# Performance work log

Measured on AMD Instinct MI355X. Metric: run time of the kernel, lower is better.

The kernel has to match this reference:

```python
import jax, jax.numpy as jnp
import numpy as np

B, S = 4, 2000            # meshes, nodes per mesh
N = B * S                  # total nodes
E = 32000                  # directed edges (before self loops)
H_TR, D_TR, FF, TOUT = 4, 64, 2048, 16
HID, HEADS, HC = 512, 6, 512
DEFORM_IN, NUM_LOOP = 7, 3


def setup_inputs():
    key = jax.random.key(0)
    ks = iter(jax.random.split(key, 64))
    def W(shape):
        return jax.random.normal(next(ks), shape, jnp.float32) / np.sqrt(shape[-1])
    inp = {}
    inp['conv_feat'] = jax.random.normal(next(ks), (B, 1), jnp.float32)
    inp['mesh_feat'] = jax.random.normal(next(ks), (N, 4), jnp.float32)
    inp['x'] = jax.random.normal(next(ks), (N, DEFORM_IN), jnp.float32)
    inp['edge_index'] = jax.random.randint(next(ks), (2, E), 0, N, jnp.int32)
    inp['embed_w'] = W((D_TR, 4)); inp['embed_b'] = jnp.zeros((D_TR,), jnp.float32)
    inp['in_proj_w'] = W((3 * D_TR, D_TR)); inp['in_proj_b'] = jnp.zeros((3 * D_TR,), jnp.float32)
    inp['out_proj_w'] = W((D_TR, D_TR)); inp['out_proj_b'] = jnp.zeros((D_TR,), jnp.float32)
    inp['ln1_g'] = jnp.ones((D_TR,), jnp.float32); inp['ln1_b'] = jnp.zeros((D_TR,), jnp.float32)
    inp['ln2_g'] = jnp.ones((D_TR,), jnp.float32); inp['ln2_b'] = jnp.zeros((D_TR,), jnp.float32)
    inp['ff1_w'] = W((FF, D_TR)); inp['ff1_b'] = jnp.zeros((FF,), jnp.float32)
    inp['ff2_w'] = W((D_TR, FF)); inp['ff2_b'] = jnp.zeros((D_TR,), jnp.float32)
    inp['tout_w'] = W((TOUT, D_TR)); inp['tout_b'] = jnp.zeros((TOUT,), jnp.float32)
    all_feat = DEFORM_IN - 2 + TOUT  # 21
    inp['lin_w'] = W((HID, all_feat)); inp['lin_b'] = jnp.zeros((HID,), jnp.float32)
    gin = 2 + HID  # 514
    inp['gat_wl'] = W((HEADS * HC, gin)); inp['gat_bl'] = jnp.zeros((HEADS * HC,), jnp.float32)
    inp['gat_wr'] = W((HEADS * HC, gin)); inp['gat_br'] = jnp.zeros((HEADS * HC,), jnp.float32)
    inp['gat_att'] = jax.random.normal(next(ks), (HEADS, HC), jnp.float32) / np.sqrt(HC)
    inp['gat_bias'] = jnp.zeros((HC,), jnp.float32)
    inp['coord1_w'] = W((HID // 2, HID)); inp['coord1_b'] = jnp.zeros((HID // 2,), jnp.float32)
    inp['coord2_w'] = W((2, HID // 2)); inp['coord2_b'] = jnp.zeros((2,), jnp.float32)
    return inp


def _ln(h, g, b):
    m = jnp.mean(h, -1, keepdims=True)
    v = jnp.var(h, -1, keepdims=True)
    return (h - m) / jnp.sqrt(v + 1e-5) * g + b


def _mrt_forward(conv_feat, mesh_feat, x, edge_index, embed_w, embed_b, in_proj_w, in_proj_b,
                 out_proj_w, out_proj_b, ln1_g, ln1_b, ln2_g, ln2_b, ff1_w, ff1_b, ff2_w, ff2_b,
                 tout_w, tout_b, lin_w, lin_b, gat_wl, gat_bl, gat_wr, gat_br, gat_att, gat_bias,
                 coord1_w, coord1_b, coord2_w, coord2_b):
    bsz = conv_feat.shape[0]
    feat_dim = mesh_feat.shape[-1]
    # ---- transformer encoder (1 post-norm layer, eval mode => no dropout) ----
    h = mesh_feat.reshape(bsz, -1, feat_dim) @ embed_w.T + embed_b  # [B,S,D]
    qkv = h @ in_proj_w.T + in_proj_b
    q, k, v = jnp.split(qkv, 3, axis=-1)
    dh = D_TR // H_TR
    hd = lambda t: t.reshape(bsz, -1, H_TR, dh)
    attn = jax.nn.softmax(jnp.einsum('bqhd,bkhd->bhqk', hd(q), hd(k)) / np.sqrt(dh), axis=-1)
    o = jnp.einsum('bhqk,bkhd->bqhd', attn, hd(v)).reshape(bsz, -1, D_TR)
    h = _ln(h + (o @ out_proj_w.T + out_proj_b), ln1_g, ln1_b)
    ff = jax.nn.relu(h @ ff1_w.T + ff1_b) @ ff2_w.T + ff2_b
    h = _ln(h + ff, ln2_g, ln2_b)
    feats = (h @ tout_w.T + tout_b).reshape(-1, TOUT)               # [N,16]
    feats = jnp.concatenate([x[:, 2:], feats], axis=1)             # [N,21]
    hidden = jax.nn.selu(feats @ lin_w.T + lin_b)                  # [N,512]
    # ---- recurrent GATv2 deformer loop ----
    coord = x[:, :2]
    n = x.shape[0]
    loops = jnp.arange(n, dtype=edge_index.dtype)                  # self loops (GATv2Conv default)
    src = jnp.concatenate([edge_index[0], loops])
    dst = jnp.concatenate([edge_index[1], loops])
    for _ in range(NUM_LOOP):
        inp = jnp.concatenate([coord, hidden], axis=1)             # [N,514]
        xl = (inp @ gat_wl.T + gat_bl).reshape(n, HEADS, HC)
        xr = (inp @ gat_wr.T + gat_br).reshape(n, HEADS, HC)
        e = jax.nn.leaky_relu(xl[src] + xr[dst], 0.2)              # [Etot,H,C]
        logits = jnp.einsum('ehc,hc->eh', e, gat_att)              # [Etot,H]
        mx = jax.ops.segment_max(logits, dst, num_segments=n)
        a = jnp.exp(logits - mx[dst])
        a = a / jax.ops.segment_sum(a, dst, num_segments=n)[dst]   # softmax per dst node
        agg = jax.ops.segment_sum(xl[src] * a[:, :, None], dst, num_segments=n)  # [N,H,C]
        hidden = jax.nn.selu(jnp.mean(agg, axis=1) + gat_bias)     # concat=False => head mean
        coord = jax.nn.selu(hidden @ coord1_w.T + coord1_b) @ coord2_w.T + coord2_b
    return coord


def reference(conv_feat, mesh_feat, x, edge_index, embed_w, embed_b, in_proj_w, in_proj_b,
              out_proj_w, out_proj_b, ln1_g, ln1_b, ln2_g, ln2_b, ff1_w, ff1_b, ff2_w, ff2_b,
              tout_w, tout_b, lin_w, lin_b, gat_wl, gat_bl, gat_wr, gat_br, gat_att, gat_bias,
              coord1_w, coord1_b, coord2_w, coord2_b):
    return _mrt_forward(conv_feat, mesh_feat, x, edge_index, embed_w, embed_b, in_proj_w, in_proj_b,
                        out_proj_w, out_proj_b, ln1_g, ln1_b, ln2_g, ln2_b, ff1_w, ff1_b, ff2_w, ff2_b,
                        tout_w, tout_b, lin_w, lin_b, gat_wl, gat_bl, gat_wr, gat_br, gat_att, gat_bias,
                        coord1_w, coord1_b, coord2_w, coord2_b)
```

## Files before the change

### kernel.cpp

```cpp
#include <hip/hip_runtime.h>
#include <hip/hip_bf16.h>
#include <math.h>

#define NN     8000
#define MPAD   8064
#define BATCH  4
#define SEQ    2000
#define DTR    64
#define NHTR   4
#define DHD    16
#define FFD    2048
#define TOUTD  16
#define HIDD   512
#define NHEADS 6
#define HCD    512
#define GIND   514
#define GOUT   3072
#define GOUT2  6144
#define NEDGE  32000
#define ELOOP  40000

#define K1     576
#define K2     1152

#define KSPLIT 20
#define KCH    100

#define CDIV(a,b) (((a)+(b)-1)/(b))

using bf16x8 = __attribute__((__ext_vector_type__(8))) __bf16;
using f32x4  = __attribute__((__ext_vector_type__(4))) float;

__device__ __forceinline__ float selu_f(float x){
  const float a = 1.6732632423543772848f;
  const float s = 1.0507009873554805f;
  return x > 0.f ? s * x : s * a * (__expf(x) - 1.f);
}

__device__ __forceinline__ unsigned short f2bf_rn(float x){
  unsigned u = __float_as_uint(x);
  unsigned r = (u + 0x7fffu + ((u >> 16) & 1u)) >> 16;
  return (unsigned short)r;
}
__device__ __forceinline__ float bf2f(unsigned short h){
  return __uint_as_float((unsigned)h << 16);
}

template<int ACT>
__global__ __launch_bounds__(256) void k_gemm(const float* __restrict__ A,
    const float* __restrict__ W, const float* __restrict__ bias,
    float* __restrict__ C, int M, int N, int K)
{
  __shared__ float As[16][68];
  __shared__ float Ws[16][68];
  const int tid = threadIdx.x;
  const int bm = blockIdx.y * 64, bn = blockIdx.x * 64;
  const int tx = tid & 15, ty = tid >> 4;
  float acc[4][4] = {};
  for (int k0 = 0; k0 < K; k0 += 16){
    #pragma unroll
    for (int i = 0; i < 4; ++i){
      int el = tid + (i << 8);
      int kk = el & 15, r = el >> 4;
      int gk = k0 + kk;
      int gm = bm + r;
      As[kk][r] = (gm < M && gk < K) ? A[(size_t)gm * K + gk] : 0.f;
      int gn = bn + r;
      Ws[kk][r] = (gn < N && gk < K) ? W[(size_t)gn * K + gk] : 0.f;
    }
    __syncthreads();
    #pragma unroll
    for (int kk = 0; kk < 16; ++kk){
      float av[4], wv[4];
      #pragma unroll
      for (int i = 0; i < 4; ++i) av[i] = As[kk][ty*4+i];
      #pragma unroll
      for (int j = 0; j < 4; ++j) wv[j] = Ws[kk][tx*4+j];
      #pragma unroll
      for (int i = 0; i < 4; ++i)
        #pragma unroll
        for (int j = 0; j < 4; ++j) acc[i][j] = fmaf(av[i], wv[j], acc[i][j]);
    }
    __syncthreads();
  }
  #pragma unroll
  for (int i = 0; i < 4; ++i){
    int gm = bm + ty*4 + i;
    if (gm >= M) continue;
    #pragma unroll
    for (int j = 0; j < 4; ++j){
      int gn = bn + tx*4 + j;
      if (gn >= N) continue;
      float v = acc[i][j] + bias[gn];
      if (ACT == 1) v = fmaxf(v, 0.f);
      if (ACT == 2) v = selu_f(v);
      C[(size_t)gm * N + gn] = v;
    }
  }
}

__global__ __launch_bounds__(256) void k_gemm_sk(const float* __restrict__ A,
    const float* __restrict__ W, float* __restrict__ part,
    int M, int N, int K, int kchunk)
{
  __shared__ float As[16][68];
  __shared__ float Ws[16][68];
  const int tid = threadIdx.x;
  const int bm = blockIdx.y * 64, bn = blockIdx.x * 64;
  const int kbeg = blockIdx.z * kchunk;
  const int tx = tid & 15, ty = tid >> 4;
  float acc[4][4] = {};
  for (int k0 = kbeg; k0 < kbeg + kchunk; k0 += 16){
    #pragma unroll
    for (int i = 0; i < 4; ++i){
      int el = tid + (i << 8);
      int kk = el & 15, r = el >> 4;
      int gk = k0 + kk;
      int gm = bm + r;
      As[kk][r] = (gm < M && gk < K) ? A[(size_t)gm * K + gk] : 0.f;
      int gn = bn + r;
      Ws[kk][r] = (gn < N && gk < K) ? W[(size_t)gn * K + gk] : 0.f;
    }
    __syncthreads();
    #pragma unroll
    for (int kk = 0; kk < 16; ++kk){
      float av[4], wv[4];
      #pragma unroll
      for (int i = 0; i < 4; ++i) av[i] = As[kk][ty*4+i];
      #pragma unroll
      for (int j = 0; j < 4; ++j) wv[j] = Ws[kk][tx*4+j];
      #pragma unroll
      for (int i = 0; i < 4; ++i)
        #pragma unroll
        for (int j = 0; j < 4; ++j) acc[i][j] = fmaf(av[i], wv[j], acc[i][j]);
    }
    __syncthreads();
  }
  float* pz = part + (size_t)blockIdx.z * M * N;
  #pragma unroll
  for (int i = 0; i < 4; ++i){
    int gm = bm + ty*4 + i;
    if (gm >= M) continue;
    #pragma unroll
    for (int j = 0; j < 4; ++j){
      int gn = bn + tx*4 + j;
      if (gn >= N) continue;
      pz[(size_t)gm * N + gn] = acc[i][j];
    }
  }
}

__global__ __launch_bounds__(256) void k_addln8(const float* __restrict__ x,
    const float* __restrict__ part, const float* __restrict__ bias,
    const float* __restrict__ g, const float* __restrict__ b,
    float* __restrict__ out)
{
  int row = blockIdx.x * 4 + (threadIdx.x >> 6);
  int lane = threadIdx.x & 63;
  if (row >= NN) return;
  float y = bias[lane];
  #pragma unroll
  for (int z = 0; z < 8; ++z) y += part[(size_t)z*NN*DTR + (size_t)row*64 + lane];
  float v = x[(size_t)row*64 + lane] + y;
  float s1 = v, s2 = v * v;
  #pragma unroll
  for (int o = 32; o; o >>= 1){ s1 += __shfl_xor(s1, o); s2 += __shfl_xor(s2, o); }
  float mean = s1 * (1.f/64.f);
  float var  = s2 * (1.f/64.f) - mean * mean;
  float r = rsqrtf(var + 1e-5f);
  out[(size_t)row*64 + lane] = (v - mean) * r * g[lane] + b[lane];
}

__global__ __launch_bounds__(256) void k_coord2(const float* __restrict__ c1,
    const float* __restrict__ w2, const float* __restrict__ b2,
    float* __restrict__ out, short* __restrict__ abf)
{
  int n = blockIdx.x, t = threadIdx.x;
  float v = c1[(size_t)n*256 + t];
  float d0 = v * w2[t], d1 = v * w2[256 + t];
  #pragma unroll
  for (int o = 32; o; o >>= 1){ d0 += __shfl_xor(d0, o); d1 += __shfl_xor(d1, o); }
  __shared__ float red[8];
  int wv = t >> 6;
  if ((t & 63) == 0){ red[wv] = d0; red[4 + wv] = d1; }
  __syncthreads();
  if (t < 2){
    float c = (t == 0 ? red[0]+red[1]+red[2]+red[3] + b2[0]
                      : red[4]+red[5]+red[6]+red[7] + b2[1]);
    out[(size_t)n*2 + t] = c;
    abf[(size_t)n*K2 + t] = (short)f2bf_rn(c);
  }
}

__global__ void k_cvt_w(const float* __restrict__ W, short* __restrict__ Wbf)
{
  int i = blockIdx.x * blockDim.x + threadIdx.x;
  if (i >= GOUT * K1) return;
  int n = i / K1, k = i - K1 * n;
  float v = (k < GIND) ? W[(size_t)n * GIND + k] : 0.f;
  Wbf[i] = (short)f2bf_rn(v);
}

__global__ void k_cvt_wc(const float* __restrict__ W, short* __restrict__ Wbf)
{
  int i = blockIdx.x * blockDim.x + threadIdx.x;
  if (i >= 256 * K1) return;
  int n = i / K1, k = i - K1 * n;
  float v = (k >= 2 && k < GIND) ? W[(size_t)n * HIDD + (k - 2)] : 0.f;
  Wbf[i] = (short)f2bf_rn(v);
}

__global__ void k_cvt_a(const float* __restrict__ coord,
                        const float* __restrict__ hidden,
                        short* __restrict__ Abf)
{
  int i = blockIdx.x * blockDim.x + threadIdx.x;
  if (i >= MPAD * K1) return;
  int n = i / K1, k = i - K1 * n;
  float v = 0.f;
  if (n < NN && k < GIND)
    v = (k < 2) ? coord[(size_t)n*2 + k] : hidden[(size_t)n*HIDD + k - 2];
  Abf[(size_t)n * K2 + k] = (short)f2bf_rn(v);
}

__global__ void k_wfuse(const float* __restrict__ ipw, const float* __restrict__ ipb,
                        const float* __restrict__ ew, const float* __restrict__ eb,
                        float* __restrict__ Wp, float* __restrict__ bp)
{
  int c = blockIdx.x * blockDim.x + threadIdx.x;
  if (c >= 192) return;
  float w4[4] = {0.f, 0.f, 0.f, 0.f};
  float bb = 0.f;
  for (int d = 0; d < 64; ++d){
    float wq = ipw[c*64 + d];
    #pragma unroll
    for (int j = 0; j < 4; ++j) w4[j] = fmaf(wq, ew[d*4 + j], w4[j]);
    bb = fmaf(wq, eb[d], bb);
  }
  #pragma unroll
  for (int j = 0; j < 4; ++j) Wp[c*4 + j] = w4[j];
  bp[c] = bb + ipb[c];
}

__global__ __launch_bounds__(256) void k_embqkv(const float* __restrict__ mesh,
    const float* __restrict__ ew, const float* __restrict__ eb,
    const float* __restrict__ Wp, const float* __restrict__ bp,
    float* __restrict__ h, float* __restrict__ qkv)
{
  int n = blockIdx.x, t = threadIdx.x;
  float m0 = mesh[n*4+0], m1 = mesh[n*4+1], m2 = mesh[n*4+2], m3 = mesh[n*4+3];
  if (t < 64){
    const float* wr = ew + t*4;
    h[(size_t)n*64 + t] =
      fmaf(m0, wr[0], fmaf(m1, wr[1], fmaf(m2, wr[2], m3*wr[3]))) + eb[t];
  } else {
    int c = t - 64;
    const float* wr = Wp + c*4;
    qkv[(size_t)n*192 + c] =
      fmaf(m0, wr[0], fmaf(m1, wr[1], fmaf(m2, wr[2], m3*wr[3]))) + bp[c];
  }
}

__global__ __launch_bounds__(256) void k_gat_mfma(
    const short* __restrict__ Abf, const short* __restrict__ Wbf,
    const float* __restrict__ bl, const float* __restrict__ br,
    unsigned short* __restrict__ Cb)
{
  __shared__ __align__(16) short smem[2 * 128 * 64];
  short* As = smem;
  short* Bs = smem + 128 * 64;
  const int tid  = threadIdx.x;
  int lin = blockIdx.y * 48 + blockIdx.x;
  int xcd = lin & 7;
  int idx = lin >> 3;
  int nb  = xcd * 6 + idx % 6;
  int mb  = idx / 6;
  const int bm = mb * 128, bn = nb * 128;
  const int w    = tid >> 6, lane = tid & 63;
  const int wr   = w >> 1, wc = w & 1;
  const int lrow = lane & 15;

  f32x4 acc[4][4];
  #pragma unroll
  for (int i = 0; i < 4; ++i)
    #pragma unroll
    for (int j = 0; j < 4; ++j) acc[i][j] = (f32x4){0.f, 0.f, 0.f, 0.f};

  for (int kt = 0; kt < 9; ++kt){
    int koff = kt * 64;
    __syncthreads();
    #pragma unroll
    for (int i = 0; i < 4; ++i){
      int l  = i * 256 + tid;
      int r  = l >> 3, j = l & 7;
      int js = j ^ (r & 7);
      const short* ga = Abf + (size_t)(bm + r) * K2 + koff + js * 8;
      const short* gb = Wbf + (size_t)(bn + r) * K1 + koff + js * 8;
      short* la = As + ((i * 256 + w * 64) << 3);
      short* lb = Bs + ((i * 256 + w * 64) << 3);
      __builtin_amdgcn_global_load_lds(
          (const __attribute__((address_space(1))) unsigned*)ga,
          (__attribute__((address_space(3))) unsigned*)la, 16, 0, 0);
      __builtin_amdgcn_global_load_lds(
          (const __attribute__((address_space(1))) unsigned*)gb,
          (__attribute__((address_space(3))) unsigned*)lb, 16, 0, 0);
    }
    __syncthreads();
    #pragma unroll
    for (int ks = 0; ks < 2; ++ks){
      const int co = ((ks * 4 + (lane >> 4)) ^ (lrow & 7)) * 8;
      bf16x8 fa[4], fb[4];
      #pragma unroll
      for (int mi = 0; mi < 4; ++mi)
        fa[mi] = *(const bf16x8*)&As[(wr*64 + mi*16 + lrow) * 64 + co];
      #pragma unroll
      for (int ni = 0; ni < 4; ++ni)
        fb[ni] = *(const bf16x8*)&Bs[(wc*64 + ni*16 + lrow) * 64 + co];
      #pragma unroll
      for (int mi = 0; mi < 4; ++mi)
        #pragma unroll
        for (int ni = 0; ni < 4; ++ni)
          acc[mi][ni] = __builtin_amdgcn_mfma_f32_16x16x32_bf16(
              fa[mi], fb[ni], acc[mi][ni], 0, 0, 0);
    }
  }
  __syncthreads();
  unsigned short* Ct = (unsigned short*)smem;
  #pragma unroll
  for (int mi = 0; mi < 4; ++mi){
    #pragma unroll
    for (int ni = 0; ni < 4; ++ni){
      int col = wc*64 + ni*16 + lrow;
      int gn  = bn + col;
      float bv = (gn < GOUT) ? bl[gn] : br[gn - GOUT];
      #pragma unroll
      for (int j = 0; j < 4; ++j){
        int row  = wr*64 + mi*16 + (lane >> 4)*4 + j;
        int colp = col ^ (((row >> 2) & 3) << 4);
        Ct[row*128 + colp] = f2bf_rn(acc[mi][ni][j] + bv);
      }
    }
  }
  __syncthreads();
  #pragma unroll
  for (int c = 0; c < 8; ++c){
    int g   = c*256 + tid;
    int row = g >> 4, cc = g & 15;
    int ccp = cc ^ (((row >> 2) & 3) << 1);
    int gm  = bm + row;
    if (gm < NN){
      bf16x8 v = *(const bf16x8*)&Ct[row*128 + ccp*8];
      *(bf16x8*)&Cb[(size_t)gm * GOUT2 + bn + cc*8] = v;
    }
  }
}

__global__ __launch_bounds__(256) void k_c1_mfma(
    const short* __restrict__ Abf, const short* __restrict__ Wbf,
    const float* __restrict__ c1b, float* __restrict__ C)
{
  __shared__ __align__(16) short smem[2 * 128 * 64];
  short* As = smem;
  short* Bs = smem + 128 * 64;
  const int tid  = threadIdx.x;
  const int bm = blockIdx.y * 128, bn = blockIdx.x * 128;
  const int w    = tid >> 6, lane = tid & 63;
  const int wr   = w >> 1, wc = w & 1;
  const int lrow = lane & 15;

  f32x4 acc[4][4];
  #pragma unroll
  for (int i = 0; i < 4; ++i)
    #pragma unroll
    for (int j = 0; j < 4; ++j) acc[i][j] = (f32x4){0.f, 0.f, 0.f, 0.f};

  for (int kt = 0; kt < 9; ++kt){
    int koff = kt * 64;
    __syncthreads();
    #pragma unroll
    for (int i = 0; i < 4; ++i){
      int l  = i * 256 + tid;
      int r  = l >> 3, j = l & 7;
      int js = j ^ (r & 7);
      const short* ga = Abf + (size_t)(bm + r) * K2 + koff + js * 8;
      const short* gb = Wbf + (size_t)(bn + r) * K1 + koff + js * 8;
      short* la = As + ((i * 256 + w * 64) << 3);
      short* lb = Bs + ((i * 256 + w * 64) << 3);
      __builtin_amdgcn_global_load_lds(
          (const __attribute__((address_space(1))) unsigned*)ga,
          (__attribute__((address_space(3))) unsigned*)la, 16, 0, 0);
      __builtin_amdgcn_global_load_lds(
          (const __attribute__((address_space(1))) unsigned*)gb,
          (__attribute__((address_space(3))) unsigned*)lb, 16, 0, 0);
    }
    __syncthreads();
    #pragma unroll
    for (int ks = 0; ks < 2; ++ks){
      const int co = ((ks * 4 + (lane >> 4)) ^ (lrow & 7)) * 8;
      bf16x8 fa[4], fb[4];
      #pragma unroll
      for (int mi = 0; mi < 4; ++mi)
        fa[mi] = *(const bf16x8*)&As[(wr*64 + mi*16 + lrow) * 64 + co];
      #pragma unroll
      for (int ni = 0; ni < 4; ++ni)
        fb[ni] = *(const bf16x8*)&Bs[(wc*64 + ni*16 + lrow) * 64 + co];
      #pragma unroll
      for (int mi = 0; mi < 4; ++mi)
        #pragma unroll
        for (int ni = 0; ni < 4; ++ni)
          acc[mi][ni] = __builtin_amdgcn_mfma_f32_16x16x32_bf16(
              fa[mi], fb[ni], acc[mi][ni], 0, 0, 0);
    }
  }
  #pragma unroll
  for (int mi = 0; mi < 4; ++mi){
    #pragma unroll
    for (int ni = 0; ni < 4; ++ni){
      int gn = bn + wc*64 + ni*16 + lrow;
      float bv = c1b[gn];
      #pragma unroll
      for (int j = 0; j < 4; ++j){
        int gm = bm + wr*64 + mi*16 + (lane >> 4) * 4 + j;
        if (gm < NN)
          C[(size_t)gm * 256 + gn] = selu_f(acc[mi][ni][j] + bv);
      }
    }
  }
}

__global__ __launch_bounds__(128) void k_attn_part(const float* __restrict__ qkv,
    float* __restrict__ Pm, float* __restrict__ Pl, float* __restrict__ Pacc)
{
  __shared__ float Ks[KCH][DHD];
  __shared__ float Vs[KCH][DHD];
  const int q1 = blockIdx.x * 128 + threadIdx.x;
  const int q2 = q1 + 1024;
  const int bh = blockIdx.y;
  const int b  = bh >> 2, h = bh & 3;
  const int ks = blockIdx.z;
  const bool v2 = q2 < SEQ;
  const float SC = 0.25f * 1.4426950408889634f;
  float qv1[DHD], qv2[DHD];
  {
    const float4* qr = (const float4*)(qkv + ((size_t)(b*SEQ + q1))*192 + h*DHD);
    #pragma unroll
    for (int j = 0; j < 4; ++j){
      float4 t = qr[j];
      qv1[j*4+0] = t.x; qv1[j*4+1] = t.y; qv1[j*4+2] = t.z; qv1[j*4+3] = t.w;
    }
  }
  if (v2){
    const float4* qr = (const float4*)(qkv + ((size_t)(b*SEQ + q2))*192 + h*DHD);
    #pragma unroll
    for (int j = 0; j < 4; ++j){
      float4 t = qr[j];
      qv2[j*4+0] = t.x; qv2[j*4+1] = t.y; qv2[j*4+2] = t.z; qv2[j*4+3] = t.w;
    }
  } else {
    #pragma unroll
    for (int j = 0; j < DHD; ++j) qv2[j] = 0.f;
  }
  const int kbeg = ks * KCH;
  for (int el = threadIdx.x; el < KCH * 4; el += 128){
    int r = el >> 2, d4 = el & 3;
    const float4* base = (const float4*)(qkv + ((size_t)(b*SEQ + kbeg + r))*192 + h*DHD);
    ((float4*)Ks[r])[d4] = base[16 + d4];
    ((float4*)Vs[r])[d4] = base[32 + d4];
  }
  __syncthreads();
  float m1 = -1e30f, l1 = 0.f, a1[DHD] = {};
  float m2 = -1e30f, l2 = 0.f, a2[DHD] = {};
  for (int r = 0; r < KCH; ++r){
    float s1 = 0.f, s2 = 0.f;
    #pragma unroll
    for (int d = 0; d < DHD; ++d){
      float kd = Ks[r][d];
      s1 = fmaf(qv1[d], kd, s1);
      s2 = fmaf(qv2[d], kd, s2);
    }
    s1 *= SC; s2 *= SC;
    if (__any((s1 > m1 + 8.f) || (s2 > m2 + 8.f))){
      float mn1 = fmaxf(m1, s1), mn2 = fmaxf(m2, s2);
      float c1 = exp2f(m1 - mn1), c2 = exp2f(m2 - mn2);
      l1 *= c1; l2 *= c2;
      #pragma unroll
      for (int d = 0; d < DHD; ++d){ a1[d] *= c1; a2[d] *= c2; }
      m1 = mn1; m2 = mn2;
    }
    float p1 = exp2f(s1 - m1), p2 = exp2f(s2 - m2);
    l1 += p1; l2 += p2;
    #pragma unroll
    for (int d = 0; d < DHD; ++d){
      float vd = Vs[r][d];
      a1[d] = fmaf(p1, vd, a1[d]);
      a2[d] = fmaf(p2, vd, a2[d]);
    }
  }
  {
    size_t qi = ((size_t)bh * SEQ + q1) * KSPLIT + ks;
    Pm[qi] = m1; Pl[qi] = l1;
    #pragma unroll
    for (int d = 0; d < DHD; ++d) Pacc[qi*DHD + d] = a1[d];
  }
  if (v2){
    size_t qi = ((size_t)bh * SEQ + q2) * KSPLIT + ks;
    Pm[qi] = m2; Pl[qi] = l2;
    #pragma unroll
    for (int d = 0; d < DHD; ++d) Pacc[qi*DHD + d] = a2[d];
  }
}

__global__ void k_attn_comb(const float* __restrict__ Pm, const float* __restrict__ Pl,
                            const float* __restrict__ Pacc, float* __restrict__ o)
{
  int qi = blockIdx.x * blockDim.x + threadIdx.x;
  if (qi >= BATCH * NHTR * SEQ) return;
  float m = -1e30f;
  #pragma unroll
  for (int ks = 0; ks < KSPLIT; ++ks) m = fmaxf(m, Pm[(size_t)qi*KSPLIT + ks]);
  float l = 0.f, acc[DHD] = {};
  #pragma unroll
  for (int ks = 0; ks < KSPLIT; ++ks){
    size_t p = (size_t)qi*KSPLIT + ks;
    float sc = exp2f(Pm[p] - m);
    l += Pl[p] * sc;
    #pragma unroll
    for (int d = 0; d < DHD; ++d) acc[d] = fmaf(Pacc[p*DHD + d], sc, acc[d]);
  }
  int bh = qi / SEQ, q = qi - bh * SEQ;
  int b = bh >> 2, h = bh & 3;
  float inv = 1.f / l;
  #pragma unroll
  for (int d = 0; d < DHD; ++d)
    o[((size_t)(b*SEQ + q))*64 + h*DHD + d] = acc[d] * inv;
}

__global__ __launch_bounds__(256) void k_addln(const float* __restrict__ x,
    const float* __restrict__ y, const float* __restrict__ g,
    const float* __restrict__ b, float* __restrict__ out)
{
  int row = blockIdx.x * 4 + (threadIdx.x >> 6);
  int lane = threadIdx.x & 63;
  if (row >= NN) return;
  float v = x[(size_t)row*64 + lane] + y[(size_t)row*64 + lane];
  float s1 = v, s2 = v * v;
  #pragma unroll
  for (int o = 32; o; o >>= 1){ s1 += __shfl_xor(s1, o); s2 += __shfl_xor(s2, o); }
  float mean = s1 * (1.f/64.f);
  float var  = s2 * (1.f/64.f) - mean * mean;
  float r = rsqrtf(var + 1e-5f);
  out[(size_t)row*64 + lane] = (v - mean) * r * g[lane] + b[lane];
}

__global__ void k_prep(const float* __restrict__ x, const float* __restrict__ tout,
                       float* __restrict__ feats, float* __restrict__ coord)
{
  int i = blockIdx.x * blockDim.x + threadIdx.x;
  if (i >= NN * 23) return;
  int n = i / 23, c = i - 23*n;
  if (c < 21)
    feats[(size_t)n*21 + c] = (c < 5) ? x[(size_t)n*7 + 2 + c] : tout[(size_t)n*16 + c - 5];
  else
    coord[(size_t)n*2 + (c - 21)] = x[(size_t)n*7 + (c - 21)];
}

__global__ void k_count(const int* __restrict__ dst, int* __restrict__ cnt)
{
  int e = blockIdx.x * blockDim.x + threadIdx.x;
  if (e >= ELOOP) return;
  int d = (e < NEDGE) ? dst[e] : e - NEDGE;
  atomicAdd(&cnt[d], 1);
}

__global__ __launch_bounds__(1024) void k_scan(const int* __restrict__ cnt,
                                               int* __restrict__ ptr)
{
  __shared__ int part[1024];
  int tid = threadIdx.x;
  const int per = 8;
  int loc[per]; int s = 0;
  int base = tid * per;
  #pragma unroll
  for (int i = 0; i < per; ++i){
    int v = (base + i < NN) ? cnt[base + i] : 0;
    loc[i] = s; s += v;
  }
  part[tid] = s;
  __syncthreads();
  for (int off = 1; off < 1024; off <<= 1){
    int v = 0;
    if (tid >= off) v = part[tid - off];
    __syncthreads();
    if (tid >= off) part[tid] += v;
    __syncthreads();
  }
  int pre = tid ? part[tid - 1] : 0;
  #pragma unroll
  for (int i = 0; i < per; ++i)
    if (base + i < NN) ptr[base + i] = pre + loc[i];
  if (tid == 1023) ptr[NN] = part[1023];
}

__global__ void k_fill(const int* __restrict__ dst, const int* __restrict__ ptr,
                       int* __restrict__ fil, int* __restrict__ eid)
{
  int e = blockIdx.x * blockDim.x + threadIdx.x;
  if (e >= ELOOP) return;
  int d = (e < NEDGE) ? dst[e] : e - NEDGE;
  int pos = ptr[d] + atomicAdd(&fil[d], 1);
  eid[pos] = e;
}

__global__ __launch_bounds__(256) void k_logits(const unsigned short* __restrict__ xc,
    const int* __restrict__ src_a, const int* __restrict__ dst_a,
    const int* __restrict__ eid, const float* __restrict__ att,
    float* __restrict__ logits2)
{
  int bid = blockIdx.x;
  int wgs = (bid & 7) * 1250 + (bid >> 3);
  int pos = wgs * 4 + (threadIdx.x >> 6);
  if (pos >= ELOOP) return;
  int lane = threadIdx.x & 63;
  int e = eid[pos];
  int s = (e < NEDGE) ? src_a[e] : e - NEDGE;
  int d = (e < NEDGE) ? dst_a[e] : e - NEDGE;
  const uint4* pl = (const uint4*)(xc + (size_t)s * GOUT2);
  const uint4* pr = (const uint4*)(xc + (size_t)d * GOUT2 + GOUT);
  const float4* pa = (const float4*)att;
  #pragma unroll 2
  for (int h = 0; h < NHEADS; ++h){
    uint4 ua = pl[h*64 + lane];
    uint4 ub = pr[h*64 + lane];
    float4 w0 = pa[h*128 + lane*2], w1 = pa[h*128 + lane*2 + 1];
    float acc = 0.f;
    auto pair = [&](unsigned a, unsigned b, float wl, float wh){
      float vl = __uint_as_float(a << 16)        + __uint_as_float(b << 16);
      float vh = __uint_as_float(a & 0xffff0000u)+ __uint_as_float(b & 0xffff0000u);
      vl = vl > 0.f ? vl : 0.2f * vl;
      vh = vh > 0.f ? vh : 0.2f * vh;
      acc = fmaf(vl, wl, acc);
      acc = fmaf(vh, wh, acc);
    };
    pair(ua.x, ub.x, w0.x, w0.y);
    pair(ua.y, ub.y, w0.z, w0.w);
    pair(ua.z, ub.z, w1.x, w1.y);
    pair(ua.w, ub.w, w1.z, w1.w);
    #pragma unroll
    for (int o2 = 32; o2; o2 >>= 1) acc += __shfl_xor(acc, o2);
    if (lane == 0) logits2[pos*NHEADS + h] = acc;
  }
}

__global__ void k_stats(const float* __restrict__ logits2, const int* __restrict__ ptr,
                        float* __restrict__ mx, float* __restrict__ inv)
{
  int i = blockIdx.x * blockDim.x + threadIdx.x;
  if (i >= NN * NHEADS) return;
  int n = i / NHEADS, h = i - NHEADS * n;
  int s0 = ptr[n], s1 = ptr[n + 1];
  float m = -1e30f;
  for (int t = s0; t < s1; ++t) m = fmaxf(m, logits2[t*NHEADS + h]);
  float s = 0.f;
  for (int t = s0; t < s1; ++t) s += __expf(logits2[t*NHEADS + h] - m);
  mx[i] = m; inv[i] = 1.f / s;
}

__global__ __launch_bounds__(256) void k_agg(const unsigned short* __restrict__ xc,
    const float* __restrict__ logits2, const float* __restrict__ mx,
    const float* __restrict__ inv, const int* __restrict__ ptr,
    const int* __restrict__ eid, const int* __restrict__ src_a,
    const float* __restrict__ gbias, float* __restrict__ hidden,
    short* __restrict__ abf)
{
  const int n = blockIdx.x;
  const int tid = threadIdx.x;
  __shared__ float a_sh[64 * NHEADS];
  __shared__ int src_sh[64];
  const int s0 = ptr[n];
  const int deg = ptr[n + 1] - s0;
  float acc[12] = {};
  for (int base = 0; base < deg; base += 64){
    int cnt = min(64, deg - base);
    __syncthreads();
    for (int t = tid; t < cnt * NHEADS; t += 256){
      int ei = t / NHEADS, h = t - NHEADS * ei;
      a_sh[t] = __expf(logits2[(s0 + base + ei)*NHEADS + h] - mx[n*NHEADS + h])
                * inv[n*NHEADS + h];
      if (h == 0){
        int e = eid[s0 + base + ei];
        src_sh[ei] = (e < NEDGE) ? src_a[e] : e - NEDGE;
      }
    }
    __syncthreads();
    for (int i2 = 0; i2 < cnt; ++i2){
      const unsigned* row = (const unsigned*)(xc + (size_t)src_sh[i2] * GOUT2);
      #pragma unroll
      for (int k = 0; k < NHEADS; ++k){
        unsigned u = row[tid + (k << 8)];
        float wgt = a_sh[i2*NHEADS + k];
        acc[2*k]   = fmaf(__uint_as_float(u << 16),         wgt, acc[2*k]);
        acc[2*k+1] = fmaf(__uint_as_float(u & 0xffff0000u), wgt, acc[2*k+1]);
      }
    }
  }
  float m0 = (acc[0]+acc[2]+acc[4]+acc[6]+acc[8]+acc[10]) * (1.f/6.f);
  float m1 = (acc[1]+acc[3]+acc[5]+acc[7]+acc[9]+acc[11]) * (1.f/6.f);
  float2 out;
  out.x = selu_f(m0 + gbias[2*tid]);
  out.y = selu_f(m1 + gbias[2*tid + 1]);
  *(float2*)&hidden[(size_t)n*HIDD + 2*tid] = out;
  unsigned short h0 = f2bf_rn(out.x), h1 = f2bf_rn(out.y);
  *(unsigned*)&abf[(size_t)n*K2 + 2 + 2*tid] = (unsigned)h0 | ((unsigned)h1 << 16);
}

extern "C" void kernel_launch(void* const* d_in, const int* in_sizes, int n_in,
                              void* d_out, int out_size, void* d_ws, size_t ws_size,
                              hipStream_t stream)
{
  const float* mesh     = (const float*)d_in[1];
  const float* xin      = (const float*)d_in[2];
  const int*   ei       = (const int*)d_in[3];
  const float* embed_w  = (const float*)d_in[4];
  const float* embed_b  = (const float*)d_in[5];
  const float* in_proj_w= (const float*)d_in[6];
  const float* in_proj_b= (const float*)d_in[7];
  const float* out_proj_w=(const float*)d_in[8];
  const float* out_proj_b=(const float*)d_in[9];
  const float* ln1_g    = (const float*)d_in[10];
  const float* ln1_b    = (const float*)d_in[11];
  const float* ln2_g    = (const float*)d_in[12];
  const float* ln2_b    = (const float*)d_in[13];
  const float* ff1_w    = (const float*)d_in[14];
  const float* ff1_b    = (const float*)d_in[15];
  const float* ff2_w    = (const float*)d_in[16];
  const float* ff2_b    = (const float*)d_in[17];
  const float* tout_w   = (const float*)d_in[18];
  const float* tout_b   = (const float*)d_in[19];
  const float* lin_w    = (const float*)d_in[20];
  const float* lin_b    = (const float*)d_in[21];
  const float* gat_wl   = (const float*)d_in[22];
  const float* gat_bl   = (const float*)d_in[23];
  const float* gat_wr   = (const float*)d_in[24];
  const float* gat_br   = (const float*)d_in[25];
  const float* gat_att  = (const float*)d_in[26];
  const float* gat_bias = (const float*)d_in[27];
  const float* coord1_w = (const float*)d_in[28];
  const float* coord1_b = (const float*)d_in[29];
  const float* coord2_w = (const float*)d_in[30];
  const float* coord2_b = (const float*)d_in[31];

  const int* esrc = ei;
  const int* edst = ei + NEDGE;

  char* ws = (char*)d_ws;
  size_t off = 0;
  auto alloc = [&](size_t nbytes){
    size_t o = off; off += (nbytes + 255) & ~(size_t)255; return o;
  };
  float* hidden = (float*)(ws + alloc((size_t)NN * HIDD * 4));
  float* coord  = (float*)(ws + alloc((size_t)NN * 2 * 4));
  unsigned short* xc = (unsigned short*)(ws + alloc((size_t)NN * GOUT2 * 2));
  float* logits = (float*)(ws + alloc((size_t)ELOOP * NHEADS * 4));
  float* mxb    = (float*)(ws + alloc((size_t)NN * NHEADS * 4));
  float* invb   = (float*)(ws + alloc((size_t)NN * NHEADS * 4));
  int*   ptr    = (int*)(ws + alloc((size_t)(NN + 1) * 4));
  int*   eid    = (int*)(ws + alloc((size_t)ELOOP * 4));
  int*   cnt    = (int*)(ws + alloc((size_t)NN * 4));
  int*   fil    = (int*)(ws + alloc((size_t)NN * 4));
  short* abf    = (short*)(ws + alloc((size_t)MPAD * K2 * 2));
  short* wlbf   = (short*)(ws + alloc((size_t)GOUT * K1 * 2));
  short* wrbf   = (short*)(ws + alloc((size_t)GOUT * K1 * 2));
  short* wcb    = (short*)(ws + alloc((size_t)256 * K1 * 2));
  float* c1     = (float*)(ws + alloc((size_t)NN * 256 * 4));
  float* Wp     = (float*)(ws + alloc((size_t)192 * 4 * 4));
  float* bp     = (float*)(ws + alloc((size_t)192 * 4));

  char* arena = (char*)xc;
  float* h       = (float*)(arena + ((size_t)0  << 20));
  float* o       = (float*)(arena + ((size_t)2  << 20));
  float* tmp     = (float*)(arena + ((size_t)4  << 20));
  float* feats   = (float*)(arena + ((size_t)6  << 20));
  float* toutb   = (float*)(arena + ((size_t)7  << 20));
  float* qkv     = (float*)(arena + ((size_t)8  << 20));
  float* Pm      = (float*)(arena + ((size_t)15 << 20));
  float* Pl      = (float*)(arena + ((size_t)18 << 20));
  float* Pacc    = (float*)(arena + ((size_t)21 << 20));
  float* part_f2 = (float*)(arena + ((size_t)8  << 20));
  float* ffmid   = (float*)(arena + ((size_t)28 << 20));

  k_wfuse<<<1, 192, 0, stream>>>(in_proj_w, in_proj_b, embed_w, embed_b, Wp, bp);
  k_embqkv<<<NN, 256, 0, stream>>>(mesh, embed_w, embed_b, Wp, bp, h, qkv);
  k_attn_part<<<dim3(CDIV(SEQ,256), BATCH*NHTR, KSPLIT), 128, 0, stream>>>(qkv, Pm, Pl, Pacc);
  k_attn_comb<<<CDIV(BATCH*NHTR*SEQ, 256), 256, 0, stream>>>(Pm, Pl, Pacc, o);
  k_gemm<0><<<dim3(1, CDIV(NN,64)), 256, 0, stream>>>(o, out_proj_w, out_proj_b, tmp, NN, 64, 64);
  k_addln<<<CDIV(NN,4), 256, 0, stream>>>(h, tmp, ln1_g, ln1_b, h);
  k_gemm<1><<<dim3(CDIV(FFD,64), CDIV(NN,64)), 256, 0, stream>>>(h, ff1_w, ff1_b, ffmid, NN, FFD, DTR);
  k_gemm_sk<<<dim3(1, CDIV(NN,64), 8), 256, 0, stream>>>(ffmid, ff2_w, part_f2, NN, DTR, FFD, 256);
  k_addln8<<<CDIV(NN,4), 256, 0, stream>>>(h, part_f2, ff2_b, ln2_g, ln2_b, h);
  k_gemm<0><<<dim3(1, CDIV(NN,64)), 256, 0, stream>>>(h, tout_w, tout_b, toutb, NN, TOUTD, DTR);
  k_prep<<<CDIV(NN*23, 256), 256, 0, stream>>>(xin, toutb, feats, coord);
  k_gemm<2><<<dim3(CDIV(HIDD,64), CDIV(NN,64)), 256, 0, stream>>>(feats, lin_w, lin_b, hidden, NN, HIDD, 21);

  hipMemsetAsync(cnt, 0, (size_t)NN * 4, stream);
  hipMemsetAsync(fil, 0, (size_t)NN * 4, stream);
  k_count<<<CDIV(ELOOP, 256), 256, 0, stream>>>(edst, cnt);
  k_scan<<<1, 1024, 0, stream>>>(cnt, ptr);
  k_fill<<<CDIV(ELOOP, 256), 256, 0, stream>>>(edst, ptr, fil, eid);
  k_cvt_w<<<CDIV(GOUT*K1, 256), 256, 0, stream>>>(gat_wl, wlbf);
  k_cvt_w<<<CDIV(GOUT*K1, 256), 256, 0, stream>>>(gat_wr, wrbf);
  k_cvt_wc<<<CDIV(256*K1, 256), 256, 0, stream>>>(coord1_w, wcb);
  k_cvt_a<<<CDIV(MPAD*K1, 256), 256, 0, stream>>>(coord, hidden, abf);

  for (int it = 0; it < 3; ++it){
    k_gat_mfma<<<dim3(48, 63), 256, 0, stream>>>(abf, wlbf, gat_bl, gat_br, xc);
    k_logits<<<ELOOP/4, 256, 0, stream>>>(xc, esrc, edst, eid, gat_att, logits);
    k_stats<<<CDIV(NN*NHEADS, 256), 256, 0, stream>>>(logits, ptr, mxb, invb);
    k_agg<<<NN, 256, 0, stream>>>(xc, logits, mxb, invb, ptr, eid, esrc, gat_bias, hidden, abf);
    k_c1_mfma<<<dim3(2, 63), 256, 0, stream>>>(abf, wcb, coord1_b, c1);
    float* cdst = (it == 2) ? (float*)d_out : coord;
    k_coord2<<<NN, 256, 0, stream>>>(c1, coord2_w, coord2_b, cdst, abf);
  }
}
```

Measured before the change: 869.7 us.

## Move transformer feed-forward GEMMs to bf16 MFMA with bf16 intermediate

Replaces the fp32 SIMT FF1 and split-K FF2 GEMMs with bf16 MFMA kernels. The weights and the layer-norm output are converted to bf16, and the 8000x2048 intermediate is stored in bf16 rather than fp32. FF2 now uses 4 K-splits instead of 8, and the add+layernorm reduction is adjusted to match. This targets the FLOP and bandwidth cost of the FF block, at the price of bf16 rounding error and a few extra conversion kernels. In FF2 only half of the waves write output, because the output width of 64 is padded to 128.

```diff
diff --git a/kernel.cpp b/kernel.cpp
--- a/kernel.cpp
+++ b/kernel.cpp
@@ -99,58 +99,7 @@
   }
 }
 
-__global__ __launch_bounds__(256) void k_gemm_sk(const float* __restrict__ A,
-    const float* __restrict__ W, float* __restrict__ part,
-    int M, int N, int K, int kchunk)
-{
-  __shared__ float As[16][68];
-  __shared__ float Ws[16][68];
-  const int tid = threadIdx.x;
-  const int bm = blockIdx.y * 64, bn = blockIdx.x * 64;
-  const int kbeg = blockIdx.z * kchunk;
-  const int tx = tid & 15, ty = tid >> 4;
-  float acc[4][4] = {};
-  for (int k0 = kbeg; k0 < kbeg + kchunk; k0 += 16){
-    #pragma unroll
-    for (int i = 0; i < 4; ++i){
-      int el = tid + (i << 8);
-      int kk = el & 15, r = el >> 4;
-      int gk = k0 + kk;
-      int gm = bm + r;
-      As[kk][r] = (gm < M && gk < K) ? A[(size_t)gm * K + gk] : 0.f;
-      int gn = bn + r;
-      Ws[kk][r] = (gn < N && gk < K) ? W[(size_t)gn * K + gk] : 0.f;
-    }
-    __syncthreads();
-    #pragma unroll
-    for (int kk = 0; kk < 16; ++kk){
-      float av[4], wv[4];
-      #pragma unroll
-      for (int i = 0; i < 4; ++i) av[i] = As[kk][ty*4+i];
-      #pragma unroll
-      for (int j = 0; j < 4; ++j) wv[j] = Ws[kk][tx*4+j];
-      #pragma unroll
-      for (int i = 0; i < 4; ++i)
-        #pragma unroll
-        for (int j = 0; j < 4; ++j) acc[i][j] = fmaf(av[i], wv[j], acc[i][j]);
-    }
-    __syncthreads();
-  }
-  float* pz = part + (size_t)blockIdx.z * M * N;
-  #pragma unroll
-  for (int i = 0; i < 4; ++i){
-    int gm = bm + ty*4 + i;
-    if (gm >= M) continue;
-    #pragma unroll
-    for (int j = 0; j < 4; ++j){
-      int gn = bn + tx*4 + j;
-      if (gn >= N) continue;
-      pz[(size_t)gm * N + gn] = acc[i][j];
-    }
-  }
-}
-
-__global__ __launch_bounds__(256) void k_addln8(const float* __restrict__ x,
+__global__ __launch_bounds__(256) void k_addln4(const float* __restrict__ x,
     const float* __restrict__ part, const float* __restrict__ bias,
     const float* __restrict__ g, const float* __restrict__ b,
     float* __restrict__ out)
@@ -160,7 +109,7 @@
   if (row >= NN) return;
   float y = bias[lane];
   #pragma unroll
-  for (int z = 0; z < 8; ++z) y += part[(size_t)z*NN*DTR + (size_t)row*64 + lane];
+  for (int z = 0; z < 4; ++z) y += part[(size_t)z*NN*DTR + (size_t)row*64 + lane];
   float v = x[(size_t)row*64 + lane] + y;
   float s1 = v, s2 = v * v;
   #pragma unroll
@@ -208,6 +157,29 @@
   int n = i / K1, k = i - K1 * n;
   float v = (k >= 2 && k < GIND) ? W[(size_t)n * HIDD + (k - 2)] : 0.f;
   Wbf[i] = (short)f2bf_rn(v);
+}
+
+__global__ void k_cvt_w1(const float* __restrict__ W, short* __restrict__ Wbf)
+{
+  int i = blockIdx.x * blockDim.x + threadIdx.x;
+  if (i >= FFD * 64) return;
+  Wbf[i] = (short)f2bf_rn(W[i]);
+}
+
+__global__ void k_cvt_w2(const float* __restrict__ W, short* __restrict__ Wbf)
+{
+  int i = blockIdx.x * blockDim.x + threadIdx.x;
+  if (i >= 128 * FFD) return;
+  int n = i / FFD;
+  Wbf[i] = (short)f2bf_rn(n < 64 ? W[i] : 0.f);
+}
+
+__global__ void k_cvt_h(const float* __restrict__ h, short* __restrict__ hbf)
+{
+  int i = blockIdx.x * blockDim.x + threadIdx.x;
+  if (i >= MPAD * 64) return;
+  int n = i >> 6;
+  hbf[i] = (short)f2bf_rn(n < NN ? h[i] : 0.f);
 }
 
 __global__ void k_cvt_a(const float* __restrict__ coord,
@@ -423,6 +395,166 @@
         int gm = bm + wr*64 + mi*16 + (lane >> 4) * 4 + j;
         if (gm < NN)
           C[(size_t)gm * 256 + gn] = selu_f(acc[mi][ni][j] + bv);
+      }
+    }
+  }
+}
+
+__global__ __launch_bounds__(256) void k_ff1_mfma(
+    const short* __restrict__ hbf, const short* __restrict__ w1b,
+    const float* __restrict__ b1, unsigned short* __restrict__ Cb)
+{
+  __shared__ __align__(16) short smem[2 * 128 * 64];
+  short* As = smem;
+  short* Bs = smem + 128 * 64;
+  const int tid  = threadIdx.x;
+  const int bm = blockIdx.y * 128, bn = blockIdx.x * 128;
+  const int w    = tid >> 6, lane = tid & 63;
+  const int wr   = w >> 1, wc = w & 1;
+  const int lrow = lane & 15;
+
+  f32x4 acc[4][4];
+  #pragma unroll
+  for (int i = 0; i < 4; ++i)
+    #pragma unroll
+    for (int j = 0; j < 4; ++j) acc[i][j] = (f32x4){0.f, 0.f, 0.f, 0.f};
+
+  #pragma unroll
+  for (int i = 0; i < 4; ++i){
+    int l  = i * 256 + tid;
+    int r  = l >> 3, j = l & 7;
+    int js = j ^ (r & 7);
+    const short* ga = hbf + (size_t)(bm + r) * 64 + js * 8;
+    const short* gb = w1b + (size_t)(bn + r) * 64 + js * 8;
+    short* la = As + ((i * 256 + w * 64) << 3);
+    short* lb = Bs + ((i * 256 + w * 64) << 3);
+    __builtin_amdgcn_global_load_lds(
+        (const __attribute__((address_space(1))) unsigned*)ga,
+        (__attribute__((address_space(3))) unsigned*)la, 16, 0, 0);
+    __builtin_amdgcn_global_load_lds(
+        (const __attribute__((address_space(1))) unsigned*)gb,
+        (__attribute__((address_space(3))) unsigned*)lb, 16, 0, 0);
+  }
+  __syncthreads();
+  #pragma unroll
+  for (int ks = 0; ks < 2; ++ks){
+    const int co = ((ks * 4 + (lane >> 4)) ^ (lrow & 7)) * 8;
+    bf16x8 fa[4], fb[4];
+    #pragma unroll
+    for (int mi = 0; mi < 4; ++mi)
+      fa[mi] = *(const bf16x8*)&As[(wr*64 + mi*16 + lrow) * 64 + co];
+    #pragma unroll
+    for (int ni = 0; ni < 4; ++ni)
+      fb[ni] = *(const bf16x8*)&Bs[(wc*64 + ni*16 + lrow) * 64 + co];
+    #pragma unroll
+    for (int mi = 0; mi < 4; ++mi)
+      #pragma unroll
+      for (int ni = 0; ni < 4; ++ni)
+        acc[mi][ni] = __builtin_amdgcn_mfma_f32_16x16x32_bf16(
+            fa[mi], fb[ni], acc[mi][ni], 0, 0, 0);
+  }
+  __syncthreads();
+  unsigned short* Ct = (unsigned short*)smem;
+  #pragma unroll
+  for (int mi = 0; mi < 4; ++mi){
+    #pragma unroll
+    for (int ni = 0; ni < 4; ++ni){
+      int col = wc*64 + ni*16 + lrow;
+      int gn  = bn + col;
+      float bv = b1[gn];
+      #pragma unroll
+      for (int j = 0; j < 4; ++j){
+        int row  = wr*64 + mi*16 + (lane >> 4)*4 + j;
+        int colp = col ^ (((row >> 2) & 3) << 4);
+        Ct[row*128 + colp] = f2bf_rn(fmaxf(acc[mi][ni][j] + bv, 0.f));
+      }
+    }
+  }
+  __syncthreads();
+  #pragma unroll
+  for (int c = 0; c < 8; ++c){
+    int g   = c*256 + tid;
+    int row = g >> 4, cc = g & 15;
+    int ccp = cc ^ (((row >> 2) & 3) << 1);
+    int gm  = bm + row;
+    if (gm < NN){
+      bf16x8 v = *(const bf16x8*)&Ct[row*128 + ccp*8];
+      *(bf16x8*)&Cb[(size_t)gm * FFD + bn + cc*8] = v;
+    }
+  }
+}
+
+__global__ __launch_bounds__(256) void k_ff2_mfma(
+    const unsigned short* __restrict__ ffb, const short* __restrict__ w2b,
+    float* __restrict__ part)
+{
+  __shared__ __align__(16) short smem[2 * 128 * 64];
+  short* As = smem;
+  short* Bs = smem + 128 * 64;
+  const int tid  = threadIdx.x;
+  const int bm = blockIdx.y * 128;
+  const int kz = blockIdx.z;
+  const int w    = tid >> 6, lane = tid & 63;
+  const int wr   = w >> 1, wc = w & 1;
+  const int lrow = lane & 15;
+
+  f32x4 acc[4][4];
+  #pragma unroll
+  for (int i = 0; i < 4; ++i)
+    #pragma unroll
+    for (int j = 0; j < 4; ++j) acc[i][j] = (f32x4){0.f, 0.f, 0.f, 0.f};
+
+  for (int kt = 0; kt < 8; ++kt){
+    int koff = kz * 512 + kt * 64;
+    __syncthreads();
+    #pragma unroll
+    for (int i = 0; i < 4; ++i){
+      int l  = i * 256 + tid;
+      int r  = l >> 3, j = l & 7;
+      int js = j ^ (r & 7);
+      const short* ga = (const short*)ffb + (size_t)(bm + r) * FFD + koff + js * 8;
+      const short* gb = w2b + (size_t)r * FFD + koff + js * 8;
+      short* la = As + ((i * 256 + w * 64) << 3);
+      short* lb = Bs + ((i * 256 + w * 64) << 3);
+      __builtin_amdgcn_global_load_lds(
+          (const __attribute__((address_space(1))) unsigned*)ga,
+          (__attribute__((address_space(3))) unsigned*)la, 16, 0, 0);
+      __builtin_amdgcn_global_load_lds(
+          (const __attribute__((address_space(1))) unsigned*)gb,
+          (__attribute__((address_space(3))) unsigned*)lb, 16, 0, 0);
+    }
+    __syncthreads();
+    #pragma unroll
+    for (int ks = 0; ks < 2; ++ks){
+      const int co = ((ks * 4 + (lane >> 4)) ^ (lrow & 7)) * 8;
+      bf16x8 fa[4], fb[4];
+      #pragma unroll
+      for (int mi = 0; mi < 4; ++mi)
+        fa[mi] = *(const bf16x8*)&As[(wr*64 + mi*16 + lrow) * 64 + co];
+      #pragma unroll
+      for (int ni = 0; ni < 4; ++ni)
+        fb[ni] = *(const bf16x8*)&Bs[(wc*64 + ni*16 + lrow) * 64 + co];
+      #pragma unroll
+      for (int mi = 0; mi < 4; ++mi)
+        #pragma unroll
+        for (int ni = 0; ni < 4; ++ni)
+          acc[mi][ni] = __builtin_amdgcn_mfma_f32_16x16x32_bf16(
+              fa[mi], fb[ni], acc[mi][ni], 0, 0, 0);
+    }
+  }
+  if (wc == 0){
+    float* pz = part + (size_t)kz * NN * 64;
+    #pragma unroll
+    for (int mi = 0; mi < 4; ++mi){
+      #pragma unroll
+      for (int ni = 0; ni < 4; ++ni){
+        int gn = ni*16 + lrow;
+        #pragma unroll
+        for (int j = 0; j < 4; ++j){
+          int gm = bm + wr*64 + mi*16 + (lane >> 4) * 4 + j;
+          if (gm < NN)
+            pz[(size_t)gm * 64 + gn] = acc[mi][ni][j];
+        }
       }
     }
   }
@@ -771,6 +903,9 @@
   short* wlbf   = (short*)(ws + alloc((size_t)GOUT * K1 * 2));
   short* wrbf   = (short*)(ws + alloc((size_t)GOUT * K1 * 2));
   short* wcb    = (short*)(ws + alloc((size_t)256 * K1 * 2));
+  short* w1b    = (short*)(ws + alloc((size_t)FFD * 64 * 2));
+  short* w2b    = (short*)(ws + alloc((size_t)128 * FFD * 2));
+  short* hbf    = (short*)(ws + alloc((size_t)MPAD * 64 * 2));
   float* c1     = (float*)(ws + alloc((size_t)NN * 256 * 4));
   float* Wp     = (float*)(ws + alloc((size_t)192 * 4 * 4));
   float* bp     = (float*)(ws + alloc((size_t)192 * 4));
@@ -785,22 +920,12 @@
   float* Pm      = (float*)(arena + ((size_t)15 << 20));
   float* Pl      = (float*)(arena + ((size_t)18 << 20));
   float* Pacc    = (float*)(arena + ((size_t)21 << 20));
-  float* part_f2 = (float*)(arena + ((size_t)8  << 20));
-  float* ffmid   = (float*)(arena + ((size_t)28 << 20));
+  unsigned short* ffb = (unsigned short*)(arena + ((size_t)28 << 20));
+  float* part_f2 = (float*)(arena + ((size_t)62 << 20));
 
   k_wfuse<<<1, 192, 0, stream>>>(in_proj_w, in_proj_b, embed_w, embed_b, Wp, bp);
-  k_embqkv<<<NN, 256, 0, stream>>>(mesh, embed_w, embed_b, Wp, bp, h, qkv);
-  k_attn_part<<<dim3(CDIV(SEQ,256), BATCH*NHTR, KSPLIT), 128, 0, stream>>>(qkv, Pm, Pl, Pacc);
-  k_attn_comb<<<CDIV(BATCH*NHTR*SEQ, 256), 256, 0, stream>>>(Pm, Pl, Pacc, o);
-  k_gemm<0><<<dim3(1, CDIV(NN,64)), 256, 0, stream>>>(o, out_proj_w, out_proj_b, tmp, NN, 64, 64);
-  k_addln<<<CDIV(NN,4), 256, 0, stream>>>(h, tmp, ln1_g, ln1_b, h);
-  k_gemm<1><<<dim3(CDIV(FFD,64), CDIV(NN,64)), 256, 0, stream>>>(h, ff1_w, ff1_b, ffmid, NN, FFD, DTR);
-  k_gemm_sk<<<dim3(1, CDIV(NN,64), 8), 256, 0, stream>>>(ffmid, ff2_w, part_f2, NN, DTR, FFD, 256);
-  k_addln8<<<CDIV(NN,4), 256, 0, stream>>>(h, part_f2, ff2_b, ln2_g, ln2_b, h);
-  k_gemm<0><<<dim3(1, CDIV(NN,64)), 256, 0, stream>>>(h, tout_w, tout_b, toutb, NN, TOUTD, DTR);
-  k_prep<<<CDIV(NN*23, 256), 256, 0, stream>>>(xin, toutb, feats, coord);
-  k_gemm<2><<<dim3(CDIV(HIDD,64), CDIV(NN,64)), 256, 0, stream>>>(feats, lin_w, lin_b, hidden, NN, HIDD, 21);
-
+  k_cvt_w1<<<CDIV(FFD*64, 256), 256, 0, stream>>>(ff1_w, w1b);
+  k_cvt_w2<<<CDIV(128*FFD, 256), 256, 0, stream>>>(ff2_w, w2b);
   hipMemsetAsync(cnt, 0, (size_t)NN * 4, stream);
   hipMemsetAsync(fil, 0, (size_t)NN * 4, stream);
   k_count<<<CDIV(ELOOP, 256), 256, 0, stream>>>(edst, cnt);
@@ -809,6 +934,19 @@
   k_cvt_w<<<CDIV(GOUT*K1, 256), 256, 0, stream>>>(gat_wl, wlbf);
   k_cvt_w<<<CDIV(GOUT*K1, 256), 256, 0, stream>>>(gat_wr, wrbf);
   k_cvt_wc<<<CDIV(256*K1, 256), 256, 0, stream>>>(coord1_w, wcb);
+
+  k_embqkv<<<NN, 256, 0, stream>>>(mesh, embed_w, embed_b, Wp, bp, h, qkv);
+  k_attn_part<<<dim3(CDIV(SEQ,256), BATCH*NHTR, KSPLIT), 128, 0, stream>>>(qkv, Pm, Pl, Pacc);
+  k_attn_comb<<<CDIV(BATCH*NHTR*SEQ, 256), 256, 0, stream>>>(Pm, Pl, Pacc, o);
+  k_gemm<0><<<dim3(1, CDIV(NN,64)), 256, 0, stream>>>(o, out_proj_w, out_proj_b, tmp, NN, 64, 64);
+  k_addln<<<CDIV(NN,4), 256, 0, stream>>>(h, tmp, ln1_g, ln1_b, h);
+  k_cvt_h<<<CDIV(MPAD*64, 256), 256, 0, stream>>>(h, hbf);
+  k_ff1_mfma<<<dim3(16, 63), 256, 0, stream>>>(hbf, w1b, ff1_b, ffb);
+  k_ff2_mfma<<<dim3(1, 63, 4), 256, 0, stream>>>(ffb, w2b, part_f2);
+  k_addln4<<<CDIV(NN,4), 256, 0, stream>>>(h, part_f2, ff2_b, ln2_g, ln2_b, h);
+  k_gemm<0><<<dim3(1, CDIV(NN,64)), 256, 0, stream>>>(h, tout_w, tout_b, toutb, NN, TOUTD, DTR);
+  k_prep<<<CDIV(NN*23, 256), 256, 0, stream>>>(xin, toutb, feats, coord);
+  k_gemm<2><<<dim3(CDIV(HIDD,64), CDIV(NN,64)), 256, 0, stream>>>(feats, lin_w, lin_b, hidden, NN, HIDD, 21);
   k_cvt_a<<<CDIV(MPAD*K1, 256), 256, 0, stream>>>(coord, hidden, abf);
 
   for (int it = 0; it < 3; ++it){
```

Result: faster. 801.6 us (-7.8%).
